# Kernel optimization log

Measured on AMD Instinct MI355X. Metric: run time of the kernel, lower is better.

## Reference

```python
import jax, jax.numpy as jnp
import numpy as np

N = 4096
IN_CH = 256
OUT_CH = 256
NUM_REL = 8


def setup_inputs() -> dict:
    key = jax.random.key(0)
    k_x, k_a, k_e, k_w = jax.random.split(key, 4)
    x = jax.random.normal(k_x, (N, IN_CH), dtype=jnp.float32)
    A = jax.random.uniform(k_a, (N, N), dtype=jnp.float32)
    edge_type = jax.random.randint(k_e, (N, N), 0, NUM_REL, dtype=jnp.int32)
    # xavier_uniform per-relation weight [R, in, out]
    limit = np.sqrt(6.0 / (IN_CH + OUT_CH))
    weight = jax.random.uniform(k_w, (NUM_REL, IN_CH, OUT_CH), dtype=jnp.float32,
                                minval=-limit, maxval=limit)
    bias = jnp.zeros((OUT_CH,), dtype=jnp.float32)
    return {"x": x, "A": A, "edge_type": edge_type, "weight": weight, "bias": bias}


def reference(x, A, edge_type, weight, bias):
    # out = sum_r ((A * [edge_type == r]) @ x) @ W_r + bias
    num_rel = weight.shape[0]
    out = jnp.zeros((x.shape[0], weight.shape[2]), dtype=x.dtype)
    for rel in range(num_rel):  # small fixed relation count
        rel_adj = A * (edge_type == rel).astype(x.dtype)   # [N, N]
        h = rel_adj @ x                                     # [N, in]
        out = out + h @ weight[rel]                         # [N, out]
    out = out + bias
    return out
```

## Files before the change

### kernel.cpp

```cpp
#include <hip/hip_runtime.h>
#include <stdint.h>


#define NN 4096

typedef __attribute__((ext_vector_type(8)))  short s16x8;
typedef __attribute__((ext_vector_type(16))) float f32x16;
typedef __attribute__((ext_vector_type(4)))  float fx4;
typedef __attribute__((ext_vector_type(4)))  int   ix4;
typedef __attribute__((ext_vector_type(4)))  unsigned int ux4;
typedef __attribute__((ext_vector_type(4)))  _Float16 h4;

union uq { ux4 u; s16x8 s; };

__device__ __forceinline__ unsigned short f2bf(float f) {
  union { float f; unsigned int u; } v; v.f = f;
  unsigned int r = v.u + 0x7fffu + ((v.u >> 16) & 1u);
  return (unsigned short)(r >> 16);
}

__device__ __forceinline__ void gld16(const void* g, void* l) {
  __builtin_amdgcn_global_load_lds(
      (const __attribute__((address_space(1))) unsigned int*)(uintptr_t)g,
      (__attribute__((address_space(3))) unsigned int*)(uintptr_t)l, 16, 0, 0);
}

__device__ __forceinline__ unsigned packAE(float a, int e) {
  unsigned ab = __float_as_uint(a) + 0x2000u;
  unsigned ex = ab >> 23;
  int el = (int)ex - 112;
  unsigned m9 = (ab >> 14) & 0x1FFu;
  unsigned v = ((unsigned)el << 9) | m9;
  if (el <= 0) v = 0;
  return (unsigned short)(((unsigned)e << 13) | (v & 0x1FFFu));
}

__global__ void k_init(const float* __restrict__ bias, float* __restrict__ out) {
  int idx = blockIdx.x * 256 + threadIdx.x;
  out[idx] = bias[idx & 255];
}

__global__ __launch_bounds__(256, 2) void k_t(const float* __restrict__ A,
                                              const int*   __restrict__ et,
                                              unsigned short* __restrict__ Apk) {
  __shared__ unsigned int lds[64 * 129];
  const int t = threadIdx.x;
  const int ib = blockIdx.x * 32;
  const int jb = blockIdx.y * 512;
  const int jgb = blockIdx.y * 64;

#pragma unroll
  for (int u = 0; u < 16; ++u) {
    const int row = u * 2 + (t >> 7);
    const int jl  = (t & 127) * 4;
    const size_t off = (size_t)(ib + row) * NN + jb + jl;
    fx4 a = *(const fx4*)(A + off);
    ix4 e = *(const ix4*)(et + off);
    unsigned d0 = (unsigned)packAE(a.x, e.x) | ((unsigned)packAE(a.y, e.y) << 16);
    unsigned d1 = (unsigned)packAE(a.z, e.z) | ((unsigned)packAE(a.w, e.w) << 16);
    const int jg = jl >> 3;
    const int dd = ((jl & 7) >> 1);
    lds[jg * 129 + row * 4 + dd]     = d0;
    lds[jg * 129 + row * 4 + dd + 1] = d1;
  }
  __syncthreads();

  const int lane = t & 63, lh1 = (t >> 5) & 1, l31 = t & 31;
  const int wv = t >> 6;
#pragma unroll
  for (int v = 0; v < 8; ++v) {
    const int jg = (wv * 8 + v) * 2 + lh1;
    const int base = jg * 129 + l31 * 4;
    ux4 q;
    q.x = lds[base]; q.y = lds[base + 1]; q.z = lds[base + 2]; q.w = lds[base + 3];
    ((ux4*)Apk)[(size_t)(jgb + jg) * NN + ib + l31] = q;
  }
  (void)lane;
}

__global__ __launch_bounds__(256, 2) void k_y(const float* __restrict__ x,
                                              const float* __restrict__ W,
                                              unsigned short* __restrict__ yt) {
  __shared__ unsigned short Wl[128 * 256];
  const int t  = threadIdx.x;
  const int j0 = blockIdx.x * 128;
  const int o0 = blockIdx.y * 16;

  {
    const int r = t >> 5, kc = t & 31;
#pragma unroll
    for (int u = 0; u < 8; ++u) {
      const int k = kc * 8 + u;
      const fx4* wp = (const fx4*)(W + ((size_t)r * 256 + k) * 256 + o0);
      fx4 w[4] = { wp[0], wp[1], wp[2], wp[3] };
#pragma unroll
      for (int i = 0; i < 16; ++i) {
        const int row = i * 8 + r;
        const int gs  = (k >> 3) ^ (row & 7);
        Wl[row * 256 + gs * 8 + (k & 7)] = f2bf(w[i >> 2][i & 3]);
      }
    }
  }
  __syncthreads();

  const int lane = t & 63, wid = t >> 6;
  const int l15 = lane & 15, lh = lane >> 4;
  const int npb = wid * 32;

  fx4 acc[8][2];
#pragma unroll
  for (int m = 0; m < 8; ++m)
#pragma unroll
    for (int n = 0; n < 2; ++n) acc[m][n] = 0.f;

  unsigned int qb[2];
#pragma unroll
  for (int n = 0; n < 2; ++n) {
    int row = npb + n * 16 + l15;
    qb[n] = (unsigned)(row * 512 + 16 * (lh ^ (row & 3))) ^ (64u * ((row >> 2) & 1));
  }
  const char* WlB = (const char*)Wl;
  const float* xb = x + (size_t)(j0 + l15) * 256 + lh * 8;

#pragma unroll
  for (int ks = 0; ks < 8; ++ks) {
    s16x8 a[8];
#pragma unroll
    for (int m = 0; m < 8; ++m) {
      const fx4* xp = (const fx4*)(xb + (size_t)m * 16 * 256 + ks * 32);
      fx4 x0 = xp[0], x1 = xp[1];
      s16x8 av;
#pragma unroll
      for (int i = 0; i < 4; ++i) av[i] = (short)f2bf(x0[i]);
#pragma unroll
      for (int i = 0; i < 4; ++i) av[4 + i] = (short)f2bf(x1[i]);
      a[m] = av;
    }
#pragma unroll
    for (int n = 0; n < 2; ++n) {
      s16x8 b = *(const s16x8*)(WlB + (qb[n] ^ (unsigned)(ks * 64)));
#pragma unroll
      for (int m = 0; m < 8; ++m)
        acc[m][n] = __builtin_amdgcn_mfma_f32_16x16x32_bf16(a[m], b, acc[m][n], 0, 0, 0);
    }
  }

#pragma unroll
  for (int m = 0; m < 8; ++m)
#pragma unroll
    for (int n = 0; n < 2; ++n)
#pragma unroll
      for (int q = 0; q < 4; ++q) {
        int jl = m * 16 + lh * 4 + q;
        int np = npb + n * 16 + l15;
        int o  = o0 + (np >> 3);
        yt[((size_t)(j0 + jl) * 256 + o) * 8 + (np & 7)] = f2bf(acc[m][n][q]);
      }
}

__global__ __launch_bounds__(256, 3) void k_main(const unsigned short* __restrict__ Apk,
                                                 const unsigned short* __restrict__ yt,
                                                 float* __restrict__ dstF,
                                                 _Float16* __restrict__ dstH,
                                                 int usePart) {
  __shared__ ux4 Bl[3 * 1024];
  char* Bc = (char*)Bl;
  const int t = threadIdx.x, lane = t & 63, w = t >> 6;
  const int l31 = lane & 31, lh1 = lane >> 5;
  const int wm = w >> 1, wn = w & 1;
  const int i0 = blockIdx.x * 128;
  const int o0 = blockIdx.y * 128;
  const int kz = blockIdx.z;
  const int jb = kz * 256;
  const int jg0 = kz * 32;

  const ux4* pA[2];
#pragma unroll
  for (int m = 0; m < 2; ++m)
    pA[m] = (const ux4*)Apk + (size_t)jg0 * NN + i0 + wm * 64 + m * 32 + l31;

  const ux4* ytg = (const ux4*)yt;
  const ux4* pB[4];
  unsigned dOff[4];
#pragma unroll
  for (int u = 0; u < 4; ++u) {
    int slot = u * 256 + t;
    pB[u] = ytg + (size_t)(jb + (slot >> 7)) * 256 + o0 + (slot & 127);
    dOff[u] = (unsigned)(slot * 16);
  }

#define ISSUE(sq, bb, ASET) do {                                          \
    _Pragma("unroll")                                                     \
    for (int u = 0; u < 4; ++u)                                           \
      gld16(pB[u] + (size_t)(sq) * 2048, Bc + (bb) * 16384 + dOff[u]);    \
    ASET[0] = pA[0][(size_t)(sq) * NN];                                   \
    ASET[1] = pA[1][(size_t)(sq) * NN];                                   \
  } while (0)

  const unsigned shA = (unsigned)(lh1 * 16);
#define BUILD(ASET, FR) do {                                              \
    _Pragma("unroll")                                                     \
    for (int m = 0; m < 2; ++m)                                           \
      _Pragma("unroll")                                                   \
      for (int ks = 0; ks < 4; ++ks) {                                    \
        unsigned u16 = (ASET[m][ks] >> shA) & 0xFFFFu;                    \
        unsigned a16 = 0x3800u | ((u16 >> 2) & 0x7FFu);                   \
        unsigned e   = u16 >> 13;                                         \
        unsigned long long sh = (unsigned long long)a16 << ((e & 3u) << 4); \
        unsigned lo = (unsigned)sh, hi = (unsigned)(sh >> 32);            \
        bool c = e < 4;                                                   \
        ux4 q; q.x = c ? lo : 0u; q.y = c ? hi : 0u;                      \
        q.z = c ? 0u : lo; q.w = c ? 0u : hi;                             \
        FR[m][ks].u = q;                                                  \
      }                                                                   \
  } while (0)

  unsigned rB[2];
#pragma unroll
  for (int n = 0; n < 2; ++n)
    rB[n] = (unsigned)((wn * 64 + n * 32 + l31) * 16);

#define COMPUTE(bb, FR) do {                                              \
    const unsigned base = (unsigned)((bb) * 16384) + (unsigned)(lh1 * 2048); \
    _Pragma("unroll")                                                     \
    for (int ks = 0; ks < 4; ++ks) {                                      \
      uq b0, b1;                                                          \
      b0.u = *(const ux4*)(Bc + base + (unsigned)(ks * 4096) + rB[0]);    \
      b1.u = *(const ux4*)(Bc + base + (unsigned)(ks * 4096) + rB[1]);    \
      _Pragma("unroll")                                                   \
      for (int m = 0; m < 2; ++m) {                                       \
        acc[m][0] = __builtin_amdgcn_mfma_f32_32x32x16_bf16(FR[m][ks].s, b0.s, acc[m][0], 0, 0, 0); \
        acc[m][1] = __builtin_amdgcn_mfma_f32_32x32x16_bf16(FR[m][ks].s, b1.s, acc[m][1], 0, 0, 0); \
      }                                                                   \
    }                                                                     \
  } while (0)

  f32x16 acc[2][2];
#pragma unroll
  for (int m = 0; m < 2; ++m)
#pragma unroll
    for (int n = 0; n < 2; ++n) acc[m][n] = 0.f;

  ux4 aE[2], aO[2];
  uq frE[2][4], frO[2][4];

  ISSUE(0, 0, aE);
  ISSUE(1, 1, aO);

  for (int s = 0; s < 32; s += 2) {
    const int sq2 = (s + 2 < 32) ? s + 2 : 31;
    const int sq3 = (s + 3 < 32) ? s + 3 : 31;
    const int b0 = s % 3, b1 = (s + 1) % 3, b2 = (s + 2) % 3;
    asm volatile("s_waitcnt vmcnt(6)" ::: "memory");
    __builtin_amdgcn_s_barrier();
    BUILD(aE, frE);
    ISSUE(sq2, b2, aE);
    __builtin_amdgcn_s_setprio(1);
    COMPUTE(b0, frE);
    __builtin_amdgcn_s_setprio(0);
    asm volatile("s_waitcnt vmcnt(6)" ::: "memory");
    __builtin_amdgcn_s_barrier();
    BUILD(aO, frO);
    ISSUE(sq3, b0, aO);
    __builtin_amdgcn_s_setprio(1);
    COMPUTE(b1, frO);
    __builtin_amdgcn_s_setprio(0);
  }
  asm volatile("s_waitcnt vmcnt(0)" ::: "memory");

  if (usePart) {
    _Float16* pp = dstH + ((size_t)kz << 20);
#pragma unroll
    for (int m = 0; m < 2; ++m)
#pragma unroll
      for (int n = 0; n < 2; ++n)
#pragma unroll
        for (int q = 0; q < 16; ++q) {
          int gi = i0 + wm * 64 + m * 32 + (q & 3) + 8 * (q >> 2) + 4 * lh1;
          int go = o0 + wn * 64 + n * 32 + l31;
          pp[(size_t)gi * 256 + go] = (_Float16)acc[m][n][q];
        }
  } else {
#pragma unroll
    for (int m = 0; m < 2; ++m)
#pragma unroll
      for (int n = 0; n < 2; ++n)
#pragma unroll
        for (int q = 0; q < 16; ++q) {
          int gi = i0 + wm * 64 + m * 32 + (q & 3) + 8 * (q >> 2) + 4 * lh1;
          int go = o0 + wn * 64 + n * 32 + l31;
          atomicAdd(dstF + (size_t)gi * 256 + go, acc[m][n][q]);
        }
  }
#undef ISSUE
#undef BUILD
#undef COMPUTE
}

__global__ __launch_bounds__(256) void k_red(const _Float16* __restrict__ part,
                                             const float* __restrict__ bias,
                                             float* __restrict__ out) {
  int idx = blockIdx.x * 256 + threadIdx.x;
  fx4 s = *(const fx4*)(bias + ((idx << 2) & 255));
#pragma unroll
  for (int k = 0; k < 16; ++k) {
    h4 h = *(const h4*)(part + ((size_t)k << 20) + (size_t)idx * 4);
    s.x += (float)h.x; s.y += (float)h.y; s.z += (float)h.z; s.w += (float)h.w;
  }
  ((fx4*)out)[idx] = s;
}

extern "C" void kernel_launch(void* const* d_in, const int* in_sizes, int n_in,
                              void* d_out, int out_size, void* d_ws, size_t ws_size,
                              hipStream_t stream) {
  const float* x    = (const float*)d_in[0];
  const float* A    = (const float*)d_in[1];
  const int*   et   = (const int*)d_in[2];
  const float* W    = (const float*)d_in[3];
  const float* bias = (const float*)d_in[4];
  float* out = (float*)d_out;

  unsigned short* yt  = (unsigned short*)d_ws;
  unsigned short* Apk = (unsigned short*)((char*)d_ws + ((size_t)16 << 20));
  _Float16*       pp  = (_Float16*)((char*)d_ws + ((size_t)48 << 20));

  const bool usePart = ws_size >= ((size_t)80 << 20);

  k_t<<<dim3(128, 8), dim3(256), 0, stream>>>(A, et, Apk);
  k_y<<<dim3(32, 16), dim3(256), 0, stream>>>(x, W, yt);
  if (usePart) {
    k_main<<<dim3(32, 2, 16), dim3(256), 0, stream>>>(Apk, yt, out, pp, 1);
    k_red<<<dim3(1024), dim3(256), 0, stream>>>(pp, bias, out);
  } else {
    k_init<<<dim3(4096), dim3(256), 0, stream>>>(bias, out);
    k_main<<<dim3(32, 2, 16), dim3(256), 0, stream>>>(Apk, yt, out, pp, 0);
  }
}
```

Before: 149.0 us.

## Merge A-packing and x·W prep kernels into one launch; remap main grid to 1D

The two independent prep kernels (packing A/edge_type into 16-bit codes, and computing x@W_r in bf16) are combined into a single launch. Blocks below 1024 do the packing and the remaining 512 do the GEMM, sharing one 64KB LDS buffer. This removes one launch and lets both workloads run at the same time on the GPU. The main kernel grid is flattened to 1D with the K-split index in the low bits, so consecutive blocks share an output tile and read different K-slices, which changes cache locality. The merged kernel runs with the larger shared-memory footprint for both roles, which may limit occupancy for the packing blocks.

New measurement: 143.9 us. 3.4% less time.

```diff
diff --git a/kernel.cpp b/kernel.cpp
--- a/kernel.cpp
+++ b/kernel.cpp
@@ -40,51 +40,56 @@
   out[idx] = bias[idx & 255];
 }
 
-__global__ __launch_bounds__(256, 2) void k_t(const float* __restrict__ A,
-                                              const int*   __restrict__ et,
-                                              unsigned short* __restrict__ Apk) {
-  __shared__ unsigned int lds[64 * 129];
+__global__ __launch_bounds__(256, 2) void k_prep(const float* __restrict__ A,
+                                                 const int*   __restrict__ et,
+                                                 unsigned short* __restrict__ Apk,
+                                                 const float* __restrict__ x,
+                                                 const float* __restrict__ W,
+                                                 unsigned short* __restrict__ yt) {
+  __shared__ char smraw[65536];
   const int t = threadIdx.x;
-  const int ib = blockIdx.x * 32;
-  const int jb = blockIdx.y * 512;
-  const int jgb = blockIdx.y * 64;
-
-#pragma unroll
-  for (int u = 0; u < 16; ++u) {
-    const int row = u * 2 + (t >> 7);
-    const int jl  = (t & 127) * 4;
-    const size_t off = (size_t)(ib + row) * NN + jb + jl;
-    fx4 a = *(const fx4*)(A + off);
-    ix4 e = *(const ix4*)(et + off);
-    unsigned d0 = (unsigned)packAE(a.x, e.x) | ((unsigned)packAE(a.y, e.y) << 16);
-    unsigned d1 = (unsigned)packAE(a.z, e.z) | ((unsigned)packAE(a.w, e.w) << 16);
-    const int jg = jl >> 3;
-    const int dd = ((jl & 7) >> 1);
-    lds[jg * 129 + row * 4 + dd]     = d0;
-    lds[jg * 129 + row * 4 + dd + 1] = d1;
-  }
-  __syncthreads();
-
-  const int lane = t & 63, lh1 = (t >> 5) & 1, l31 = t & 31;
-  const int wv = t >> 6;
-#pragma unroll
-  for (int v = 0; v < 8; ++v) {
-    const int jg = (wv * 8 + v) * 2 + lh1;
-    const int base = jg * 129 + l31 * 4;
-    ux4 q;
-    q.x = lds[base]; q.y = lds[base + 1]; q.z = lds[base + 2]; q.w = lds[base + 3];
-    ((ux4*)Apk)[(size_t)(jgb + jg) * NN + ib + l31] = q;
-  }
-  (void)lane;
-}
-
-__global__ __launch_bounds__(256, 2) void k_y(const float* __restrict__ x,
-                                              const float* __restrict__ W,
-                                              unsigned short* __restrict__ yt) {
-  __shared__ unsigned short Wl[128 * 256];
-  const int t  = threadIdx.x;
-  const int j0 = blockIdx.x * 128;
-  const int o0 = blockIdx.y * 16;
+
+  if (blockIdx.x < 1024) {
+    unsigned int* lds = (unsigned int*)smraw;
+    const int b  = blockIdx.x;
+    const int ib = (b & 127) * 32;
+    const int byy = b >> 7;
+    const int jb = byy * 512;
+    const int jgb = byy * 64;
+
+#pragma unroll
+    for (int u = 0; u < 16; ++u) {
+      const int row = u * 2 + (t >> 7);
+      const int jl  = (t & 127) * 4;
+      const size_t off = (size_t)(ib + row) * NN + jb + jl;
+      fx4 a = *(const fx4*)(A + off);
+      ix4 e = *(const ix4*)(et + off);
+      unsigned d0 = (unsigned)packAE(a.x, e.x) | ((unsigned)packAE(a.y, e.y) << 16);
+      unsigned d1 = (unsigned)packAE(a.z, e.z) | ((unsigned)packAE(a.w, e.w) << 16);
+      const int jg = jl >> 3;
+      const int dd = ((jl & 7) >> 1);
+      lds[jg * 129 + row * 4 + dd]     = d0;
+      lds[jg * 129 + row * 4 + dd + 1] = d1;
+    }
+    __syncthreads();
+
+    const int lh1 = (t >> 5) & 1, l31 = t & 31;
+    const int wv = t >> 6;
+#pragma unroll
+    for (int v = 0; v < 8; ++v) {
+      const int jg = (wv * 8 + v) * 2 + lh1;
+      const int base = jg * 129 + l31 * 4;
+      ux4 q;
+      q.x = lds[base]; q.y = lds[base + 1]; q.z = lds[base + 2]; q.w = lds[base + 3];
+      ((ux4*)Apk)[(size_t)(jgb + jg) * NN + ib + l31] = q;
+    }
+    return;
+  }
+
+  unsigned short* Wl = (unsigned short*)smraw;
+  const int b2 = blockIdx.x - 1024;
+  const int j0 = (b2 & 31) * 128;
+  const int o0 = (b2 >> 5) * 16;
 
   {
     const int r = t >> 5, kc = t & 31;
@@ -138,10 +143,10 @@
     }
 #pragma unroll
     for (int n = 0; n < 2; ++n) {
-      s16x8 b = *(const s16x8*)(WlB + (qb[n] ^ (unsigned)(ks * 64)));
+      s16x8 bb = *(const s16x8*)(WlB + (qb[n] ^ (unsigned)(ks * 64)));
 #pragma unroll
       for (int m = 0; m < 8; ++m)
-        acc[m][n] = __builtin_amdgcn_mfma_f32_16x16x32_bf16(a[m], b, acc[m][n], 0, 0, 0);
+        acc[m][n] = __builtin_amdgcn_mfma_f32_16x16x32_bf16(a[m], bb, acc[m][n], 0, 0, 0);
     }
   }
 
@@ -168,9 +173,11 @@
   const int t = threadIdx.x, lane = t & 63, w = t >> 6;
   const int l31 = lane & 31, lh1 = lane >> 5;
   const int wm = w >> 1, wn = w & 1;
-  const int i0 = blockIdx.x * 128;
-  const int o0 = blockIdx.y * 128;
-  const int kz = blockIdx.z;
+  const int b = blockIdx.x;
+  const int kz = b & 15;
+  const int io = b >> 4;
+  const int i0 = (io >> 1) * 128;
+  const int o0 = (io & 1) * 128;
   const int jb = kz * 256;
   const int jg0 = kz * 32;
 
@@ -326,13 +333,12 @@
 
   const bool usePart = ws_size >= ((size_t)80 << 20);
 
-  k_t<<<dim3(128, 8), dim3(256), 0, stream>>>(A, et, Apk);
-  k_y<<<dim3(32, 16), dim3(256), 0, stream>>>(x, W, yt);
+  k_prep<<<dim3(1536), dim3(256), 0, stream>>>(A, et, Apk, x, W, yt);
   if (usePart) {
-    k_main<<<dim3(32, 2, 16), dim3(256), 0, stream>>>(Apk, yt, out, pp, 1);
+    k_main<<<dim3(1024), dim3(256), 0, stream>>>(Apk, yt, out, pp, 1);
     k_red<<<dim3(1024), dim3(256), 0, stream>>>(pp, bias, out);
   } else {
     k_init<<<dim3(4096), dim3(256), 0, stream>>>(bias, out);
-    k_main<<<dim3(32, 2, 16), dim3(256), 0, stream>>>(Apk, yt, out, pp, 0);
-  }
-}
+    k_main<<<dim3(1024), dim3(256), 0, stream>>>(Apk, yt, out, pp, 0);
+  }
+}
```
